# Kernel optimization log

Hardware: AMD Instinct MI355X
Metric: run time of the kernel (lower is better)

Reference implementation:

```python
import jax, jax.numpy as jnp
import numpy as np

MODEL_DIM = 1024
NUM_HEADS = 16
HEAD_DIM = MODEL_DIM // NUM_HEADS
ROPE_BASE = 10000.0


def apply_rope_full(x):
    # RoPE applied over the FULL model_dim (before head split), interleaved pairs.
    B, S, D = x.shape
    half = D // 2
    inv_freq = 1.0 / (ROPE_BASE ** (jnp.arange(half, dtype=x.dtype) / half))  # [half]
    ang = jnp.arange(S, dtype=x.dtype)[:, None] * inv_freq[None, :]           # [S, half]
    cos, sin = jnp.cos(ang), jnp.sin(ang)
    x1 = x[..., 0::2]  # [B,S,half]
    x2 = x[..., 1::2]
    r1 = x1 * cos - x2 * sin
    r2 = x1 * sin + x2 * cos
    # re-interleave
    return jnp.stack([r1, r2], axis=-1).reshape(B, S, D)


def setup_inputs() -> dict:
    key = jax.random.key(0)
    ks = jax.random.split(key, 9)
    B, S, D = 4, 2048, MODEL_DIM
    sc = 1.0 / np.sqrt(D)
    inp = {
        "X": jax.random.normal(ks[0], (B, S, D), dtype=jnp.float32),
        "Wq": jax.random.normal(ks[1], (D, D), dtype=jnp.float32) * sc,
        "bq": jnp.zeros((D,), dtype=jnp.float32),
        "Wk": jax.random.normal(ks[2], (D, D), dtype=jnp.float32) * sc,
        "bk": jnp.zeros((D,), dtype=jnp.float32),
        "Wv": jax.random.normal(ks[3], (D, D), dtype=jnp.float32) * sc,
        "bv": jnp.zeros((D,), dtype=jnp.float32),
        "Wo": jax.random.normal(ks[4], (D, D), dtype=jnp.float32) * sc,
        "bo": jnp.zeros((D,), dtype=jnp.float32),
    }
    return inp


def reference(X, Wq, bq, Wk, bk, Wv, bv, Wo, bo):
    B, S, D = X.shape
    H, hd = NUM_HEADS, HEAD_DIM
    q = apply_rope_full(X @ Wq + bq)  # [B,S,D], RoPE on full dim as in source
    k = apply_rope_full(X @ Wk + bk)
    v = X @ Wv + bv
    # split heads (contiguous slices d1:d2 == reshape to [B,S,H,hd])
    qh = q.reshape(B, S, H, hd)
    kh = k.reshape(B, S, H, hd)
    vh = v.reshape(B, S, H, hd)
    scale = 1.0 / jnp.sqrt(jnp.asarray(hd, dtype=X.dtype))
    scores = jnp.einsum("bqhd,bkhd->bhqk", qh, kh) * scale  # [B,H,S,S]
    causal = jnp.tril(jnp.ones((S, S), dtype=bool))
    scores = jnp.where(causal[None, None], scores, -jnp.inf)
    weights = jax.nn.softmax(scores, axis=-1)
    attn = jnp.einsum("bhqk,bkhd->bqhd", weights, vh).reshape(B, S, D)
    return attn @ Wo + bo
```

## Files before the change

kernel.cpp:

```cpp
#include <hip/hip_runtime.h>

typedef unsigned short u16;
typedef unsigned int   u32;
typedef __attribute__((ext_vector_type(4))) float f32x4;
typedef __attribute__((ext_vector_type(8))) short short8;

#define MODEL_DIM 1024
#define SEQ 2048
#define BATCH 4
#define NHEAD 16
#define HDIM 64
#define MTOT (BATCH*SEQ)
#define ELEMS ((size_t)MTOT*MODEL_DIM)

__device__ __forceinline__ u16 f2bf(float f) {
    u32 u = __float_as_uint(f);
    u = (u + 0x7fffu + ((u >> 16) & 1u)) >> 16;
    return (u16)u;
}
__device__ __forceinline__ u32 pack2(float a, float b) {
    return (u32)f2bf(a) | ((u32)f2bf(b) << 16);
}
__device__ __forceinline__ u32 cvtpk(float lo, float hi) {
    u32 r;
    asm("v_cvt_pk_bf16_f32 %0, %1, %2" : "=v"(r) : "v"(lo), "v"(hi));
    return r;
}
__device__ __forceinline__ float exp2a(float x) {
    float r;
    asm("v_exp_f32 %0, %1" : "=v"(r) : "v"(x));
    return r;
}

#define GLOAD16(g, l) __builtin_amdgcn_global_load_lds(                        \
        (const __attribute__((address_space(1))) unsigned int*)(g),            \
        (__attribute__((address_space(3))) unsigned int*)(l), 16, 0, 0)

__global__ __launch_bounds__(256) void prep_k(const float* __restrict__ X,
                                              u16* __restrict__ Xb,
                                              const float* __restrict__ Wq,
                                              const float* __restrict__ Wk,
                                              const float* __restrict__ Wv,
                                              const float* __restrict__ Wo,
                                              u16* __restrict__ Wt) {
    const int bid = blockIdx.x, t = threadIdx.x;
    if (bid < 8192) {
        size_t i = ((size_t)bid * 256 + t) * 4;
        float4 v = *(const float4*)(X + i);
        uint2 o; o.x = pack2(v.x, v.y); o.y = pack2(v.z, v.w);
        *(uint2*)(Xb + i) = o;
        return;
    }
    __shared__ float tile[32][33];
    const int bid2 = bid - 8192;
    const int z = bid2 >> 10, rem = bid2 & 1023;
    const int by = rem >> 5, bx = rem & 31;
    const float* W = (z == 0) ? Wq : (z == 1) ? Wk : (z == 2) ? Wv : Wo;
    const int k0 = by * 32, n0 = bx * 32;
    const int x = t & 31, y = t >> 5;
    for (int i = 0; i < 4; ++i)
        tile[y + i * 8][x] = W[(size_t)(k0 + y + i * 8) * MODEL_DIM + n0 + x];
    __syncthreads();
    u16* out = Wt + ((size_t)z << 20);
    for (int i = 0; i < 4; ++i)
        out[(size_t)(n0 + y + i * 8) * MODEL_DIM + k0 + x] = f2bf(tile[x][y + i * 8]);
}

template<int MODE>
__global__ __launch_bounds__(256) void gemm128_k(
        const u16* __restrict__ A, const u16* __restrict__ Wt,
        u16* __restrict__ Qb, u16* __restrict__ Kb, u32* __restrict__ VT,
        float* __restrict__ outO,
        const float* __restrict__ bq, const float* __restrict__ bk,
        const float* __restrict__ bv, const float* __restrict__ bo) {
    __shared__ __align__(16) u16 As[128 * 32];
    __shared__ __align__(16) u16 Bs[128 * 32];
    const int tid  = threadIdx.x;
    const int wave = tid >> 6, lane = tid & 63;
    const int l15  = lane & 15, quad = lane >> 4;
    const int wm = (wave & 1) * 64, wn = (wave >> 1) * 64;
    const int m0 = blockIdx.x * 128;
    const int n0 = blockIdx.y * 128;

    const u16* bbase;
    if (MODE == 0) {
        int region = n0 >> 10;
        bbase = Wt + ((size_t)region << 20) + (size_t)(n0 & 1023) * MODEL_DIM;
    } else {
        bbase = Wt + ((size_t)3 << 20) + (size_t)n0 * MODEL_DIM;
    }
    const u16* abase = A + (size_t)m0 * MODEL_DIM;

    f32x4 acc[4][4] = {};
    const int r0 = tid >> 2, kc0 = (tid & 3) * 8;
    const u16* ga = abase + (size_t)r0 * MODEL_DIM + kc0;
    const u16* gb = bbase + (size_t)r0 * MODEL_DIM + kc0;
    u16* la0 = &As[tid * 8];
    u16* la1 = &As[2048 + tid * 8];
    u16* lb0 = &Bs[tid * 8];
    u16* lb1 = &Bs[2048 + tid * 8];

    for (int k0 = 0; k0 < MODEL_DIM; k0 += 32) {
        GLOAD16(ga + k0, la0);
        GLOAD16(ga + (size_t)64 * MODEL_DIM + k0, la1);
        GLOAD16(gb + k0, lb0);
        GLOAD16(gb + (size_t)64 * MODEL_DIM + k0, lb1);
        __syncthreads();
        short8 af[4], bf[4];
        for (int i = 0; i < 4; ++i)
            af[i] = *(const short8*)(&As[(wm + i * 16 + l15) * 32 + quad * 8]);
        for (int i = 0; i < 4; ++i)
            bf[i] = *(const short8*)(&Bs[(wn + i * 16 + l15) * 32 + quad * 8]);
        for (int mi = 0; mi < 4; ++mi)
            for (int ni = 0; ni < 4; ++ni)
                acc[mi][ni] = __builtin_amdgcn_mfma_f32_16x16x32_bf16(
                                  af[mi], bf[ni], acc[mi][ni], 0, 0, 0);
        __syncthreads();
    }

    if (MODE == 0) {
        const int region = n0 >> 10;
        if (region < 2) {
            const float* bias = (region == 0) ? bq : bk;
            u16* dst = (region == 0) ? Qb : Kb;
            const float qsc = (region == 0) ? 0.125f * 1.44269504f : 1.0f;
            const float cfr = -0.017989922f;
            float invf[4];
            for (int ni = 0; ni < 4; ++ni) {
                int c = (n0 + wn + ni * 16 + l15) & 1023;
                invf[ni] = __expf((float)(c >> 1) * cfr);
            }
            const float sgn = (l15 & 1) ? 1.0f : -1.0f;
            for (int mi = 0; mi < 4; ++mi)
                for (int r = 0; r < 4; ++r) {
                    size_t rowg = (size_t)(m0 + wm + mi * 16 + quad * 4 + r);
                    float fs = (float)(int)(rowg & 2047);
                    for (int ni = 0; ni < 4; ++ni) {
                        int c = (n0 + wn + ni * 16 + l15) & 1023;
                        float v = acc[mi][ni][r] + bias[c];
                        float mate = __shfl_xor(v, 1, 64);
                        float sn, cs;
                        __sincosf(fs * invf[ni], &sn, &cs);
                        float o = (v * cs + sgn * mate * sn) * qsc;
                        dst[rowg * MODEL_DIM + c] = f2bf(o);
                    }
                }
        } else {
            const int b_ = m0 >> 11;
            const int s0 = m0 & 2047;
            for (int ni = 0; ni < 4; ++ni) {
                int c = (n0 & 1023) + wn + ni * 16 + l15;
                float bvc = bv[c];
                u32* vtrow = VT + (size_t)((b_ * NHEAD + (c >> 6)) * HDIM
                                           + (c & 63)) * (SEQ / 2);
                for (int mi = 0; mi < 4; ++mi) {
                    int sb = s0 + wm + mi * 16 + quad * 4;
                    uint2 w;
                    w.x = cvtpk(acc[mi][ni][0] + bvc, acc[mi][ni][1] + bvc);
                    w.y = cvtpk(acc[mi][ni][2] + bvc, acc[mi][ni][3] + bvc);
                    *(uint2*)(vtrow + (sb >> 1)) = w;
                }
            }
        }
    } else {
        for (int mi = 0; mi < 4; ++mi)
            for (int r = 0; r < 4; ++r) {
                size_t rowg = (size_t)(m0 + wm + mi * 16 + quad * 4 + r);
                for (int ni = 0; ni < 4; ++ni) {
                    int colg = n0 + wn + ni * 16 + l15;
                    outO[rowg * MODEL_DIM + colg] = acc[mi][ni][r] + bo[colg];
                }
            }
    }
}

__global__ __launch_bounds__(256, 2) void attn_k(const u16* __restrict__ Qb,
                                                 const u16* __restrict__ Kb,
                                                 const u32* __restrict__ VT32,
                                                 u16* __restrict__ Ob) {
    __shared__ __align__(16) u16 Ks[2][64 * 64];
    __shared__ __align__(16) u16 Vs[2][64 * 64];
    __shared__ __align__(16) u16 Pl[4 * 32 * 72];
    const int tid  = threadIdx.x;
    const int wave = tid >> 6, lane = tid & 63;
    const int l15  = lane & 15, quad = lane >> 4;
    const int j = blockIdx.x;
    const int h = blockIdx.y, b = blockIdx.z;
    u16* pw = &Pl[wave * 32 * 72];

    const int key0 = tid >> 3;
    const int c8   = (tid & 7) * 8;
    const int c4   = (tid & 7) * 4;
    const int lko  = key0 * 64 + (((tid & 7) ^ (key0 & 7)) * 8);
    const u16* kgp = Kb + (size_t)(b * SEQ) * MODEL_DIM + h * HDIM;
    const u32* vgp = VT32 + (size_t)((b * NHEAD + h) * HDIM) * (SEQ / 2);

    int bufc = 0;
    for (int pp = 0; pp < 2; ++pp) {
        const int qt = pp ? j : 15 - j;
        const int q0 = qt * 128;
        const int qbase = q0 + wave * 32;

        short8 qfr[2][2];
        for (int qf = 0; qf < 2; ++qf)
            for (int ks = 0; ks < 2; ++ks)
                qfr[qf][ks] = *(const short8*)(Qb
                    + (size_t)(b * SEQ + qbase + qf * 16 + l15) * MODEL_DIM
                    + h * HDIM + ks * 32 + quad * 8);

        float m_i[2] = {-1e30f, -1e30f}, l_i[2] = {0.f, 0.f};
        f32x4 o_acc[4][2] = {};

        const int nkt = (q0 + 128) >> 6;
        uint4 kr0 = *(const uint4*)(kgp + (size_t)key0 * MODEL_DIM + c8);
        uint4 kr1 = *(const uint4*)(kgp + (size_t)(key0 + 32) * MODEL_DIM + c8);
        uint4 vr0 = *(const uint4*)(vgp + (size_t)key0 * (SEQ / 2) + c4);
        uint4 vr1 = *(const uint4*)(vgp + (size_t)(key0 + 32) * (SEQ / 2) + c4);

        for (int kt = 0; kt < nkt; ++kt) {
            const int k0 = kt * 64;
            u16* ksb = Ks[bufc];
            u16* vsb = Vs[bufc];
            *(uint4*)(&ksb[lko])        = kr0;
            *(uint4*)(&ksb[lko + 2048]) = kr1;
            *(uint4*)(&vsb[lko])        = vr0;
            *(uint4*)(&vsb[lko + 2048]) = vr1;
            __syncthreads();

            if (kt + 1 < nkt) {
                const int kn = k0 + 64;
                kr0 = *(const uint4*)(kgp + (size_t)(kn + key0) * MODEL_DIM + c8);
                kr1 = *(const uint4*)(kgp + (size_t)(kn + key0 + 32) * MODEL_DIM + c8);
                vr0 = *(const uint4*)(vgp + (size_t)key0 * (SEQ / 2) + (kn >> 1) + c4);
                vr1 = *(const uint4*)(vgp + (size_t)(key0 + 32) * (SEQ / 2)
                                      + (kn >> 1) + c4);
            }

            if (k0 <= qbase + 31) {
                f32x4 s[4][2] = {};
                for (int ks = 0; ks < 2; ++ks) {
                    short8 kfr[4];
                    for (int kf = 0; kf < 4; ++kf)
                        kfr[kf] = *(const short8*)(&ksb[(kf * 16 + l15) * 64
                                      + (((ks * 4 + quad) ^ (l15 & 7)) * 8)]);
                    __builtin_amdgcn_s_setprio(1);
                    for (int kf = 0; kf < 4; ++kf)
                        for (int qf = 0; qf < 2; ++qf)
                            s[kf][qf] = __builtin_amdgcn_mfma_f32_16x16x32_bf16(
                                            kfr[kf], qfr[qf][ks], s[kf][qf], 0, 0, 0);
                    __builtin_amdgcn_s_setprio(0);
                }
                for (int qf = 0; qf < 2; ++qf) {
                    int qg = qbase + qf * 16 + l15;
                    if (k0 + 63 > qbase + qf * 16) {
                        for (int kf = 0; kf < 4; ++kf)
                            for (int r = 0; r < 4; ++r)
                                if (k0 + kf * 16 + quad * 4 + r > qg)
                                    s[kf][qf][r] = -1e30f;
                    }
                    float t0 = fmaxf(fmaxf(s[0][qf][0], s[0][qf][1]),
                                     fmaxf(s[0][qf][2], s[0][qf][3]));
                    float t1 = fmaxf(fmaxf(s[1][qf][0], s[1][qf][1]),
                                     fmaxf(s[1][qf][2], s[1][qf][3]));
                    float t2 = fmaxf(fmaxf(s[2][qf][0], s[2][qf][1]),
                                     fmaxf(s[2][qf][2], s[2][qf][3]));
                    float t3 = fmaxf(fmaxf(s[3][qf][0], s[3][qf][1]),
                                     fmaxf(s[3][qf][2], s[3][qf][3]));
                    float rmax = fmaxf(fmaxf(t0, t1), fmaxf(t2, t3));
                    rmax = fmaxf(rmax, __shfl_xor(rmax, 16, 64));
                    rmax = fmaxf(rmax, __shfl_xor(rmax, 32, 64));
                    if (!__all(rmax <= m_i[qf] + 8.0f)) {
                        float mn = fmaxf(m_i[qf], rmax);
                        float alpha = exp2a(m_i[qf] - mn);
                        m_i[qf] = mn;
                        l_i[qf] *= alpha;
                        for (int dt = 0; dt < 4; ++dt)
                            for (int r = 0; r < 4; ++r) o_acc[dt][qf][r] *= alpha;
                    }
                    float mref = m_i[qf];
                    float psum = 0.f;
                    for (int kf = 0; kf < 4; ++kf)
                        for (int r = 0; r < 4; ++r) {
                            float p = exp2a(s[kf][qf][r] - mref);
                            s[kf][qf][r] = p;
                            psum += p;
                        }
                    psum += __shfl_xor(psum, 16, 64);
                    psum += __shfl_xor(psum, 32, 64);
                    l_i[qf] += psum;
                    for (int kf = 0; kf < 4; ++kf) {
                        uint2 w;
                        w.x = cvtpk(s[kf][qf][0], s[kf][qf][1]);
                        w.y = cvtpk(s[kf][qf][2], s[kf][qf][3]);
                        *(uint2*)(&pw[(qf * 16 + l15) * 72 + kf * 16 + quad * 4]) = w;
                    }
                }
                for (int ks = 0; ks < 2; ++ks) {
                    short8 pfr[2], vfr[4];
                    for (int qf = 0; qf < 2; ++qf)
                        pfr[qf] = *(const short8*)(&pw[(qf * 16 + l15) * 72
                                                       + ks * 32 + quad * 8]);
                    for (int dt = 0; dt < 4; ++dt)
                        vfr[dt] = *(const short8*)(&vsb[(dt * 16 + l15) * 64
                                      + (((ks * 4 + quad) ^ (l15 & 7)) * 8)]);
                    __builtin_amdgcn_s_setprio(1);
                    for (int dt = 0; dt < 4; ++dt)
                        for (int qf = 0; qf < 2; ++qf)
                            o_acc[dt][qf] = __builtin_amdgcn_mfma_f32_16x16x32_bf16(
                                                vfr[dt], pfr[qf], o_acc[dt][qf], 0, 0, 0);
                    __builtin_amdgcn_s_setprio(0);
                }
            }
            bufc ^= 1;
        }

        for (int qf = 0; qf < 2; ++qf) {
            float rl = 1.f / l_i[qf];
            int q = qbase + qf * 16 + l15;
            for (int dt = 0; dt < 4; ++dt) {
                uint2 w;
                w.x = cvtpk(o_acc[dt][qf][0] * rl, o_acc[dt][qf][1] * rl);
                w.y = cvtpk(o_acc[dt][qf][2] * rl, o_acc[dt][qf][3] * rl);
                *(uint2*)(&Ob[(size_t)(b * SEQ + q) * MODEL_DIM
                              + h * HDIM + dt * 16 + quad * 4]) = w;
            }
        }
    }
}

extern "C" void kernel_launch(void* const* d_in, const int* in_sizes, int n_in,
                              void* d_out, int out_size, void* d_ws, size_t ws_size,
                              hipStream_t stream) {
    const float* X  = (const float*)d_in[0];
    const float* Wq = (const float*)d_in[1];
    const float* bq = (const float*)d_in[2];
    const float* Wk = (const float*)d_in[3];
    const float* bk = (const float*)d_in[4];
    const float* Wv = (const float*)d_in[5];
    const float* bv = (const float*)d_in[6];
    const float* Wo = (const float*)d_in[7];
    const float* bo = (const float*)d_in[8];
    float* out = (float*)d_out;

    char* ws = (char*)d_ws;
    u16* Xb   = (u16*)ws;
    u16* Ob   = (u16*)ws;
    u16* Wt   = (u16*)(ws + 16777216);
    u16* Qb   = (u16*)(ws + 25165824);
    u16* Kb   = (u16*)(ws + 41943040);
    u32* VT32 = (u32*)(ws + 75497472);

    prep_k<<<dim3(12288), dim3(256), 0, stream>>>(X, Xb, Wq, Wk, Wv, Wo, Wt);
    gemm128_k<0><<<dim3(64, 24), dim3(256), 0, stream>>>(Xb, Wt, Qb, Kb, VT32,
                                                         nullptr, bq, bk, bv, nullptr);
    attn_k<<<dim3(8, 16, 4), dim3(256), 0, stream>>>(Qb, Kb, VT32, Ob);
    gemm128_k<1><<<dim3(64, 8), dim3(256), 0, stream>>>(Ob, Wt, nullptr, nullptr,
                                                        nullptr, out,
                                                        nullptr, nullptr, nullptr, bo);
}
```

Measured before the change: 273.2 us.

## Replace QKV projection GEMM with 256x256-tile double-buffered swizzled pipelined kernel

The fused QKV projection now runs in a new 512-thread kernel with 256x256 output tiles and a K-step of 64. Its LDS tiles are double-buffered and XOR-swizzled, and global prefetch of the next stage is interleaved with MFMA phases using s_setprio and barriers. The larger tiles raise operand reuse and aim to hide load latency, at the cost of 128KB of LDS per block, higher register pressure and a grid of only 384 blocks. The output projection keeps the old 128-tile kernel, now specialised.

```diff
diff --git a/kernel.cpp b/kernel.cpp
--- a/kernel.cpp
+++ b/kernel.cpp
@@ -66,13 +66,159 @@
         out[(size_t)(n0 + y + i * 8) * MODEL_DIM + k0 + x] = f2bf(tile[x][y + i * 8]);
 }
 
-template<int MODE>
-__global__ __launch_bounds__(256) void gemm128_k(
+__global__ __launch_bounds__(512, 2) void gemm256qkv_k(
         const u16* __restrict__ A, const u16* __restrict__ Wt,
         u16* __restrict__ Qb, u16* __restrict__ Kb, u32* __restrict__ VT,
-        float* __restrict__ outO,
         const float* __restrict__ bq, const float* __restrict__ bk,
-        const float* __restrict__ bv, const float* __restrict__ bo) {
+        const float* __restrict__ bv) {
+    __shared__ __align__(16) u16 Ls[65536];
+    const int tid  = threadIdx.x;
+    const int wv   = tid >> 6, lane = tid & 63;
+    const int l15  = lane & 15, quad = lane >> 4;
+    const int wr = wv >> 2, wc = wv & 3;
+    const int bh = wc >> 1;
+    const int sb = wr * 2 + (wc & 1);
+    const int m0 = blockIdx.x * 256;
+    const int region = blockIdx.y >> 2;
+    const int n0loc = (blockIdx.y & 3) * 256;
+
+    const u16* Ag = A + (size_t)m0 * MODEL_DIM;
+    const u16* Bg = Wt + ((size_t)region << 20) + (size_t)n0loc * MODEL_DIM;
+
+    f32x4 acc[8][4] = {};
+
+#define STAGE2(kt, d, q) do {                                                  \
+    const int kk0_ = (kt) * 64;                                                \
+    { int L_ = ((q) * 256 + wc * 64 + lane) * 16;                              \
+      int P_ = L_ ^ (((L_ >> 7) & 7) << 4);                                    \
+      GLOAD16(Ag + (size_t)(wr * 128 + (P_ >> 7)) * MODEL_DIM + kk0_           \
+                 + ((P_ & 127) >> 1),                                          \
+              &Ls[(d) * 32768 + wr * 8192 + (L_ >> 1)]); }                     \
+    { int L_ = ((q) * 256 + sb * 64 + lane) * 16;                              \
+      int P_ = L_ ^ (((L_ >> 7) & 7) << 4);                                    \
+      GLOAD16(Bg + (size_t)(bh * 128 + (P_ >> 7)) * MODEL_DIM + kk0_           \
+                 + ((P_ & 127) >> 1),                                          \
+              &Ls[(d) * 32768 + 16384 + bh * 8192 + (L_ >> 1)]); }             \
+} while (0)
+
+#define LDA8(mf, ks) ({                                                        \
+    int P_ = ((mf) * 16 + l15) * 128 + ((ks) * 4 + quad) * 16;                 \
+    int L_ = P_ ^ (((P_ >> 7) & 7) << 4);                                      \
+    *(const short8*)(ab + (L_ >> 1)); })
+#define LDB8(nf, ks) ({                                                        \
+    int P_ = ((wc & 1) * 64 + (nf) * 16 + l15) * 128 + ((ks) * 4 + quad) * 16; \
+    int L_ = P_ ^ (((P_ >> 7) & 7) << 4);                                      \
+    *(const short8*)(bb2 + (L_ >> 1)); })
+
+#define PHASE_MFMA(MH)                                                         \
+    __builtin_amdgcn_s_setprio(1);                                             \
+    _Pragma("unroll")                                                          \
+    for (int j2 = 0; j2 < 4; ++j2)                                             \
+        _Pragma("unroll")                                                      \
+        for (int nf2 = 0; nf2 < 4; ++nf2)                                      \
+            acc[(MH) * 4 + j2][nf2] = __builtin_amdgcn_mfma_f32_16x16x32_bf16( \
+                af[j2], bf[nf2], acc[(MH) * 4 + j2][nf2], 0, 0, 0);            \
+    __builtin_amdgcn_s_setprio(0);
+
+    STAGE2(0, 0, 0); STAGE2(0, 0, 1); STAGE2(0, 0, 2); STAGE2(0, 0, 3);
+
+    for (int t = 0; t < 16; ++t) {
+        const int pp2 = t & 1;
+        const u16* ab  = &Ls[pp2 * 32768 + wr * 8192];
+        const u16* bb2 = &Ls[pp2 * 32768 + 16384 + bh * 8192];
+        const int dn = pp2 ^ 1;
+        const bool more = (t + 1) < 16;
+        short8 af[4], bf[4];
+        if (more) STAGE2(t + 1, dn, 0);
+        if (more) asm volatile("s_waitcnt vmcnt(2)" ::: "memory");
+        else      asm volatile("s_waitcnt vmcnt(0)" ::: "memory");
+        __builtin_amdgcn_s_barrier();
+        __builtin_amdgcn_sched_barrier(0);
+        #pragma unroll
+        for (int nf = 0; nf < 4; ++nf) bf[nf] = LDB8(nf, 0);
+        #pragma unroll
+        for (int j = 0; j < 4; ++j) af[j] = LDA8(j, 0);
+        PHASE_MFMA(0)
+        __builtin_amdgcn_s_barrier();
+        #pragma unroll
+        for (int j = 0; j < 4; ++j) af[j] = LDA8(4 + j, 0);
+        if (more) STAGE2(t + 1, dn, 1);
+        __builtin_amdgcn_s_barrier();
+        __builtin_amdgcn_sched_barrier(0);
+        PHASE_MFMA(1)
+        __builtin_amdgcn_s_barrier();
+        #pragma unroll
+        for (int nf = 0; nf < 4; ++nf) bf[nf] = LDB8(nf, 1);
+        #pragma unroll
+        for (int j = 0; j < 4; ++j) af[j] = LDA8(j, 1);
+        if (more) STAGE2(t + 1, dn, 2);
+        __builtin_amdgcn_s_barrier();
+        __builtin_amdgcn_sched_barrier(0);
+        PHASE_MFMA(0)
+        __builtin_amdgcn_s_barrier();
+        #pragma unroll
+        for (int j = 0; j < 4; ++j) af[j] = LDA8(4 + j, 1);
+        if (more) STAGE2(t + 1, dn, 3);
+        __builtin_amdgcn_s_barrier();
+        __builtin_amdgcn_sched_barrier(0);
+        PHASE_MFMA(1)
+        __builtin_amdgcn_s_barrier();
+    }
+
+    if (region < 2) {
+        const float* bias = region ? bk : bq;
+        u16* dst = region ? Kb : Qb;
+        const float qsc = region ? 1.0f : 0.125f * 1.44269504f;
+        const float cfr = -0.017989922f;
+        float invf[4];
+        #pragma unroll
+        for (int nf = 0; nf < 4; ++nf) {
+            int c = n0loc + wc * 64 + nf * 16 + l15;
+            invf[nf] = __expf((float)(c >> 1) * cfr);
+        }
+        const float sgn = (l15 & 1) ? 1.0f : -1.0f;
+        for (int mf = 0; mf < 8; ++mf)
+            for (int r = 0; r < 4; ++r) {
+                size_t rowg = (size_t)(m0 + wr * 128 + mf * 16 + quad * 4 + r);
+                float fs = (float)(int)(rowg & 2047);
+                #pragma unroll
+                for (int nf = 0; nf < 4; ++nf) {
+                    int c = n0loc + wc * 64 + nf * 16 + l15;
+                    float v = acc[mf][nf][r] + bias[c];
+                    float mate = __shfl_xor(v, 1, 64);
+                    float sn, cs;
+                    __sincosf(fs * invf[nf], &sn, &cs);
+                    float o = (v * cs + sgn * mate * sn) * qsc;
+                    dst[rowg * MODEL_DIM + c] = f2bf(o);
+                }
+            }
+    } else {
+        const int b_ = m0 >> 11;
+        const int s0 = m0 & 2047;
+        #pragma unroll
+        for (int nf = 0; nf < 4; ++nf) {
+            int c = n0loc + wc * 64 + nf * 16 + l15;
+            float bvc = bv[c];
+            u32* vtrow = VT + (size_t)((b_ * NHEAD + (c >> 6)) * HDIM
+                                       + (c & 63)) * (SEQ / 2);
+            for (int mf = 0; mf < 8; ++mf) {
+                int sb2 = s0 + wr * 128 + mf * 16 + quad * 4;
+                uint2 w;
+                w.x = cvtpk(acc[mf][nf][0] + bvc, acc[mf][nf][1] + bvc);
+                w.y = cvtpk(acc[mf][nf][2] + bvc, acc[mf][nf][3] + bvc);
+                *(uint2*)(vtrow + (sb2 >> 1)) = w;
+            }
+        }
+    }
+#undef STAGE2
+#undef LDA8
+#undef LDB8
+#undef PHASE_MFMA
+}
+
+__global__ __launch_bounds__(256) void gemm128o_k(
+        const u16* __restrict__ A, const u16* __restrict__ Wt,
+        float* __restrict__ outO, const float* __restrict__ bo) {
     __shared__ __align__(16) u16 As[128 * 32];
     __shared__ __align__(16) u16 Bs[128 * 32];
     const int tid  = threadIdx.x;
@@ -82,13 +228,7 @@
     const int m0 = blockIdx.x * 128;
     const int n0 = blockIdx.y * 128;
 
-    const u16* bbase;
-    if (MODE == 0) {
-        int region = n0 >> 10;
-        bbase = Wt + ((size_t)region << 20) + (size_t)(n0 & 1023) * MODEL_DIM;
-    } else {
-        bbase = Wt + ((size_t)3 << 20) + (size_t)n0 * MODEL_DIM;
-    }
+    const u16* bbase = Wt + ((size_t)3 << 20) + (size_t)n0 * MODEL_DIM;
     const u16* abase = A + (size_t)m0 * MODEL_DIM;
 
     f32x4 acc[4][4] = {};
@@ -118,60 +258,14 @@
         __syncthreads();
     }
 
-    if (MODE == 0) {
-        const int region = n0 >> 10;
-        if (region < 2) {
-            const float* bias = (region == 0) ? bq : bk;
-            u16* dst = (region == 0) ? Qb : Kb;
-            const float qsc = (region == 0) ? 0.125f * 1.44269504f : 1.0f;
-            const float cfr = -0.017989922f;
-            float invf[4];
+    for (int mi = 0; mi < 4; ++mi)
+        for (int r = 0; r < 4; ++r) {
+            size_t rowg = (size_t)(m0 + wm + mi * 16 + quad * 4 + r);
             for (int ni = 0; ni < 4; ++ni) {
-                int c = (n0 + wn + ni * 16 + l15) & 1023;
-                invf[ni] = __expf((float)(c >> 1) * cfr);
-            }
-            const float sgn = (l15 & 1) ? 1.0f : -1.0f;
-            for (int mi = 0; mi < 4; ++mi)
-                for (int r = 0; r < 4; ++r) {
-                    size_t rowg = (size_t)(m0 + wm + mi * 16 + quad * 4 + r);
-                    float fs = (float)(int)(rowg & 2047);
-                    for (int ni = 0; ni < 4; ++ni) {
-                        int c = (n0 + wn + ni * 16 + l15) & 1023;
-                        float v = acc[mi][ni][r] + bias[c];
-                        float mate = __shfl_xor(v, 1, 64);
-                        float sn, cs;
-                        __sincosf(fs * invf[ni], &sn, &cs);
-                        float o = (v * cs + sgn * mate * sn) * qsc;
-                        dst[rowg * MODEL_DIM + c] = f2bf(o);
-                    }
-                }
-        } else {
-            const int b_ = m0 >> 11;
-            const int s0 = m0 & 2047;
-            for (int ni = 0; ni < 4; ++ni) {
-                int c = (n0 & 1023) + wn + ni * 16 + l15;
-                float bvc = bv[c];
-                u32* vtrow = VT + (size_t)((b_ * NHEAD + (c >> 6)) * HDIM
-                                           + (c & 63)) * (SEQ / 2);
-                for (int mi = 0; mi < 4; ++mi) {
-                    int sb = s0 + wm + mi * 16 + quad * 4;
-                    uint2 w;
-                    w.x = cvtpk(acc[mi][ni][0] + bvc, acc[mi][ni][1] + bvc);
-                    w.y = cvtpk(acc[mi][ni][2] + bvc, acc[mi][ni][3] + bvc);
-                    *(uint2*)(vtrow + (sb >> 1)) = w;
-                }
+                int colg = n0 + wn + ni * 16 + l15;
+                outO[rowg * MODEL_DIM + colg] = acc[mi][ni][r] + bo[colg];
             }
         }
-    } else {
-        for (int mi = 0; mi < 4; ++mi)
-            for (int r = 0; r < 4; ++r) {
-                size_t rowg = (size_t)(m0 + wm + mi * 16 + quad * 4 + r);
-                for (int ni = 0; ni < 4; ++ni) {
-                    int colg = n0 + wn + ni * 16 + l15;
-                    outO[rowg * MODEL_DIM + colg] = acc[mi][ni][r] + bo[colg];
-                }
-            }
-    }
 }
 
 __global__ __launch_bounds__(256, 2) void attn_k(const u16* __restrict__ Qb,
@@ -351,10 +445,8 @@
     u32* VT32 = (u32*)(ws + 75497472);
 
     prep_k<<<dim3(12288), dim3(256), 0, stream>>>(X, Xb, Wq, Wk, Wv, Wo, Wt);
-    gemm128_k<0><<<dim3(64, 24), dim3(256), 0, stream>>>(Xb, Wt, Qb, Kb, VT32,
-                                                         nullptr, bq, bk, bv, nullptr);
+    gemm256qkv_k<<<dim3(32, 12), dim3(512), 0, stream>>>(Xb, Wt, Qb, Kb, VT32,
+                                                         bq, bk, bv);
     attn_k<<<dim3(8, 16, 4), dim3(256), 0, stream>>>(Qb, Kb, VT32, Ob);
-    gemm128_k<1><<<dim3(64, 8), dim3(256), 0, stream>>>(Ob, Wt, nullptr, nullptr,
-                                                        nullptr, out,
-                                                        nullptr, nullptr, nullptr, bo);
-}
+    gemm128o_k<<<dim3(64, 8), dim3(256), 0, stream>>>(Ob, Wt, out, bo);
+}
```

After: 359.6 us. +31.6%, slower.
